# Kernel optimization log

Hardware: AMD Instinct MI355X
Metric: run time of the kernel (lower is better)

The kernel has to match this reference:

```python
import jax, jax.numpy as jnp
import numpy as np

N, E, D, T, B, OUT = 20000, 80000, 768, 4, 3, 768
SCALE = 0.02


def _layer_norm(x, g, b):
    mu = jnp.mean(x, axis=-1, keepdims=True)
    var = jnp.var(x, axis=-1, keepdims=True)
    return (x - mu) / jnp.sqrt(var + 1e-5) * g + b


def _typed_linear(x, etype, bases, coeff):
    # DGL TypedLinear with basis regularizer: W[t] = sum_b coeff[t,b] * bases[b]
    # computed as 3 shared GEMMs + per-edge weighted sum (avoids [E,D,D] gather).
    c = coeff[etype]  # [E, B]
    y = c[:, 0:1] * (x @ bases[0])
    for bb in range(1, bases.shape[0]):
        y = y + c[:, bb:bb + 1] * (x @ bases[bb])
    return y


def _time_encode(t, freq, phase):
    return jnp.cos(t[:, None] * freq[None, :] + phase[None, :])


def _segment_softmax(scores, seg, n):
    m = jax.ops.segment_max(scores, seg, num_segments=n)
    m = jnp.where(jnp.isfinite(m), m, 0.0)  # empty segments -> -inf guard
    e = jnp.exp(scores - m[seg])
    den = jax.ops.segment_sum(e, seg, num_segments=n)[seg]
    return e / jnp.where(den == 0, 1.0, den)


def _forward(h, etime_hete, first_etime_homo, second_etime_homo, w_src, w_dst,
             ln_g, ln_b, src_bases, src_coeff, dst_bases, dst_coeff,
             user_bases, user_coeff, lin_w, lin_b, time_freq, time_phase,
             src_hete, dst_hete, first_etype_hete, src_homo, dst_homo,
             first_etype_homo, second_etype_homo, n_nodes):
    inv_sqrt_d = 1.0 / jnp.sqrt(jnp.asarray(768.0, h.dtype))
    n_src = h @ w_src.T  # src_weight (no bias)
    n_dst = h @ w_dst.T  # dst_weight (no bias)

    # --- heterogeneous edges ---
    sf = n_src[src_hete]
    df = n_dst[dst_hete]
    hete_src = jax.nn.relu(_typed_linear(_layer_norm(sf, ln_g, ln_b), first_etype_hete, src_bases, src_coeff))
    msg_h = _time_encode(etime_hete, time_freq, time_phase) + hete_src
    e_h = jnp.sum(msg_h * df, axis=1) * inv_sqrt_d
    a_h = _segment_softmax(e_h, dst_hete, n_nodes)
    h_hete = jax.ops.segment_sum(a_h[:, None] * msg_h, dst_hete, num_segments=n_nodes)

    # --- homogeneous edges ---
    sf = n_src[src_homo]
    df = n_dst[dst_homo]
    dst_feat = jax.nn.relu(_typed_linear(_layer_norm(df, ln_g, ln_b), first_etype_homo, dst_bases, dst_coeff))
    homo_feat = jax.nn.relu(_typed_linear(_layer_norm(sf, ln_g, ln_b), second_etype_homo, user_bases, user_coeff))
    t_homo = jnp.maximum(first_etime_homo, second_etime_homo)
    msg_o = _time_encode(t_homo, time_freq, time_phase) + homo_feat
    e_o = jnp.sum(msg_o * dst_feat, axis=1) * inv_sqrt_d
    a_o = _segment_softmax(e_o, dst_homo, n_nodes)
    h_homo = jax.ops.segment_sum(a_o[:, None] * msg_o, dst_homo, num_segments=n_nodes)

    n = jnp.concatenate([h_hete, h_homo], axis=-1)  # [N, 2D]
    z = jax.nn.relu(n @ lin_w.T + lin_b)
    zn = jnp.linalg.norm(z, axis=1, keepdims=True)
    return z / jnp.where(zn == 0, 1.0, zn)


def setup_inputs() -> dict:
    key = jax.random.key(0)
    ks = jax.random.split(key, 24)
    inp = {
        'h': jax.random.normal(ks[0], (N, D), jnp.float32),
        'etime_hete': jax.random.uniform(ks[1], (E,), jnp.float32),
        'first_etime_homo': jax.random.uniform(ks[2], (E,), jnp.float32),
        'second_etime_homo': jax.random.uniform(ks[3], (E,), jnp.float32),
        'w_src': jax.random.normal(ks[4], (D, D), jnp.float32) * SCALE,
        'w_dst': jax.random.normal(ks[5], (D, D), jnp.float32) * SCALE,
        'ln_g': jnp.ones((D,), jnp.float32),
        'ln_b': jnp.zeros((D,), jnp.float32),
        'src_bases': jax.random.normal(ks[6], (B, D, D), jnp.float32) * SCALE,
        'src_coeff': jax.random.normal(ks[7], (T, B), jnp.float32),
        'dst_bases': jax.random.normal(ks[8], (B, D, D), jnp.float32) * SCALE,
        'dst_coeff': jax.random.normal(ks[9], (T, B), jnp.float32),
        'user_bases': jax.random.normal(ks[10], (B, D, D), jnp.float32) * SCALE,
        'user_coeff': jax.random.normal(ks[11], (T, B), jnp.float32),
        'lin_w': jax.random.normal(ks[12], (OUT, 2 * D), jnp.float32) * SCALE,
        'lin_b': jnp.zeros((OUT,), jnp.float32),
        'time_freq': jnp.asarray(1.0 / 10 ** np.linspace(0, 9, D), jnp.float32),
        'time_phase': jnp.zeros((D,), jnp.float32),
        'src_hete': jax.random.randint(ks[13], (E,), 0, N, jnp.int32),
        'dst_hete': jax.random.randint(ks[14], (E,), 0, N, jnp.int32),
        'first_etype_hete': jax.random.randint(ks[15], (E,), 0, T, jnp.int32),
        'src_homo': jax.random.randint(ks[16], (E,), 0, N, jnp.int32),
        'dst_homo': jax.random.randint(ks[17], (E,), 0, N, jnp.int32),
        'first_etype_homo': jax.random.randint(ks[18], (E,), 0, T, jnp.int32),
        'second_etype_homo': jax.random.randint(ks[19], (E,), 0, T, jnp.int32),
        'num_nodes': N,
    }
    return inp


def reference(h, etime_hete, first_etime_homo, second_etime_homo, w_src, w_dst,
              ln_g, ln_b, src_bases, src_coeff, dst_bases, dst_coeff,
              user_bases, user_coeff, lin_w, lin_b, time_freq, time_phase,
              src_hete, dst_hete, first_etype_hete, src_homo, dst_homo,
              first_etype_homo, second_etype_homo, num_nodes):
    return _forward(h, etime_hete, first_etime_homo, second_etime_homo, w_src,
                    w_dst, ln_g, ln_b, src_bases, src_coeff, dst_bases,
                    dst_coeff, user_bases, user_coeff, lin_w, lin_b,
                    time_freq, time_phase, src_hete, dst_hete,
                    first_etype_hete, src_homo, dst_homo, first_etype_homo,
                    second_etype_homo, num_nodes)
```

## Files before the change

kernel.cpp:

```cpp
#include <hip/hip_runtime.h>
#include <hip/hip_bf16.h>
#include <stdint.h>

#define D 768
#define INV_SQRT_D 0.03608439182435161269f

static void* g_scratch = nullptr;
#define SCRATCH_BYTES ((size_t)600 * 1024 * 1024)

__attribute__((constructor))
static void _alloc_scratch() {
    if (hipMalloc(&g_scratch, SCRATCH_BYTES) != hipSuccess) g_scratch = nullptr;
}

static inline int cdiv(int a, int b) { return (a + b - 1) / b; }

typedef __attribute__((ext_vector_type(8))) short bf16x8;
typedef __attribute__((ext_vector_type(4))) float f32x4;

__device__ __forceinline__ unsigned cvt2b(float lo, float hi) {
    unsigned r;
    asm("v_cvt_pk_bf16_f32 %0, %1, %2" : "=v"(r) : "v"(lo), "v"(hi));
    return r;
}
__device__ __forceinline__ unsigned short f2b(float f) {
    return (unsigned short)cvt2b(f, f);
}
__device__ __forceinline__ float b2f(unsigned short u) {
    union { unsigned u; float f; } c; c.u = (unsigned)u << 16;
    return c.f;
}

__device__ __forceinline__ float block_reduce_sum(float v) {
#pragma unroll
    for (int off = 32; off > 0; off >>= 1) v += __shfl_down(v, off, 64);
    __shared__ float sm[4];
    int lane = threadIdx.x & 63, w = threadIdx.x >> 6;
    __syncthreads();
    if (lane == 0) sm[w] = v;
    __syncthreads();
    return (sm[0] + sm[1]) + (sm[2] + sm[3]);
}

template <bool CONCAT, bool BF16C, bool RELU, bool BIAS>
__global__ __launch_bounds__(256) void mfma_gemm(
    const unsigned short* __restrict__ A1, const unsigned short* __restrict__ A2,
    int lda, int ksplit,
    const unsigned short* __restrict__ B, int ldb,
    void* __restrict__ Cv, int ldc,
    const float* __restrict__ bias,
    int M, int K)
{
    __shared__ unsigned short As[128 * 64];
    __shared__ unsigned short Bs[128 * 64];
    const int tid = threadIdx.x;
    const int wv = tid >> 6, lane = tid & 63;
    const int m0 = blockIdx.y * 128, n0 = blockIdx.x * 128;
    const int wm = (wv >> 1) << 6;
    const int wn = (wv & 1) << 6;
    const int fr = lane & 15;
    const int fq = lane >> 4;

    f32x4 acc[4][4] = {};

    for (int k0 = 0; k0 < K; k0 += 64) {
        const unsigned short* Asrc = A1;
        int kk = k0;
        if (CONCAT && k0 >= ksplit) { Asrc = A2; kk = k0 - ksplit; }
#pragma unroll
        for (int j = 0; j < 4; ++j) {
            int idx = j * 256 + tid;
            int row = idx >> 3;
            int gs  = ((idx & 7) ^ (row & 7)) << 3;
            int am = m0 + row; if (am > M - 1) am = M - 1;
            const unsigned short* ga = Asrc + (size_t)am * lda + kk + gs;
            char* la = (char*)As + (size_t)(j * 256 + wv * 64) * 16;
            __builtin_amdgcn_global_load_lds(
                (const __attribute__((address_space(1))) unsigned int*)ga,
                (__attribute__((address_space(3))) unsigned int*)la, 16, 0, 0);
            const unsigned short* gb = B + (size_t)(n0 + row) * ldb + k0 + gs;
            char* lb = (char*)Bs + (size_t)(j * 256 + wv * 64) * 16;
            __builtin_amdgcn_global_load_lds(
                (const __attribute__((address_space(1))) unsigned int*)gb,
                (__attribute__((address_space(3))) unsigned int*)lb, 16, 0, 0);
        }
        __syncthreads();

#pragma unroll
        for (int ks = 0; ks < 2; ++ks) {
            bf16x8 af[4], bfv[4];
            const int gr = (((ks * 4 + fq) ^ (fr & 7)) << 3);
#pragma unroll
            for (int i = 0; i < 4; ++i) {
                af[i]  = *(const bf16x8*)&As[(wm + i * 16 + fr) * 64 + gr];
                bfv[i] = *(const bf16x8*)&Bs[(wn + i * 16 + fr) * 64 + gr];
            }
#pragma unroll
            for (int mi = 0; mi < 4; ++mi)
#pragma unroll
                for (int ni = 0; ni < 4; ++ni)
                    acc[mi][ni] = __builtin_amdgcn_mfma_f32_16x16x32_bf16(
                        af[mi], bfv[ni], acc[mi][ni], 0, 0, 0);
        }
        __syncthreads();
    }

#pragma unroll
    for (int mi = 0; mi < 4; ++mi) {
#pragma unroll
        for (int r = 0; r < 4; ++r) {
            int m = m0 + wm + mi * 16 + fq * 4 + r;
            if (m >= M) continue;
#pragma unroll
            for (int ni = 0; ni < 4; ++ni) {
                int n = n0 + wn + ni * 16 + fr;
                float v = acc[mi][ni][r];
                if (BIAS) v += bias[n];
                if (RELU) v = fmaxf(v, 0.f);
                if (BF16C) ((unsigned short*)Cv)[(size_t)m * ldc + n] = f2b(v);
                else       ((float*)Cv)[(size_t)m * ldc + n] = v;
            }
        }
    }
}

__global__ void f32_to_bf16_kernel(const float* __restrict__ in,
                                   unsigned short* __restrict__ out, int n4) {
    int i = blockIdx.x * 256 + threadIdx.x;
    if (i >= n4) return;
    float4 v = *reinterpret_cast<const float4*>(in + (size_t)i * 4);
    ushort4 o;
    o.x = f2b(v.x); o.y = f2b(v.y); o.z = f2b(v.z); o.w = f2b(v.w);
    *reinterpret_cast<ushort4*>(out + (size_t)i * 4) = o;
}

__global__ __launch_bounds__(256) void combine_transpose_kernel(
    const float* __restrict__ in, const float* __restrict__ coeff,
    unsigned short* __restrict__ out) {
    int t = blockIdx.z;
    float c0 = coeff[t * 3 + 0], c1 = coeff[t * 3 + 1], c2 = coeff[t * 3 + 2];
    __shared__ float tile[32][33];
    int bx = blockIdx.x * 32, by = blockIdx.y * 32;
    int tx = threadIdx.x & 31, ty = threadIdx.x >> 5;
#pragma unroll
    for (int i = 0; i < 32; i += 8) {
        size_t idx = (size_t)(by + ty + i) * D + bx + tx;
        tile[ty + i][tx] = c0 * in[idx] + c1 * in[idx + (size_t)D * D]
                         + c2 * in[idx + (size_t)2 * D * D];
    }
    __syncthreads();
    unsigned short* o = out + (size_t)t * D * D;
#pragma unroll
    for (int i = 0; i < 32; i += 8)
        o[(size_t)(bx + ty + i) * D + by + tx] = f2b(tile[tx][ty + i]);
}

__global__ __launch_bounds__(256) void ln_bf16_kernel(
    unsigned short* __restrict__ x, int ld,
    const float* __restrict__ g, const float* __restrict__ b)
{
    unsigned short* r = x + (size_t)blockIdx.x * ld;
    int t = threadIdx.x;
    float v0 = b2f(r[t]), v1 = b2f(r[t + 256]), v2 = b2f(r[t + 512]);
    float s = block_reduce_sum(v0 + v1 + v2);
    float mu = s * (1.f / 768.f);
    float d0 = v0 - mu, d1 = v1 - mu, d2 = v2 - mu;
    float q = block_reduce_sum(d0 * d0 + d1 * d1 + d2 * d2);
    float rstd = 1.f / sqrtf(q * (1.f / 768.f) + 1e-5f);
    r[t]       = f2b(d0 * rstd * g[t]       + b[t]);
    r[t + 256] = f2b(d1 * rstd * g[t + 256] + b[t + 256]);
    r[t + 512] = f2b(d2 * rstd * g[t + 512] + b[t + 512]);
}

__global__ void zero_int_kernel(int* __restrict__ p, int n) {
    int i = blockIdx.x * 256 + threadIdx.x;
    if (i < n) p[i] = 0;
}

__global__ void count2_kernel(const int* __restrict__ dA, const int* __restrict__ dB,
                              int* __restrict__ cntA, int* __restrict__ cntB, int E) {
    int e = blockIdx.x * 256 + threadIdx.x;
    if (e < E) {
        atomicAdd(&cntA[dA[e]], 1);
        atomicAdd(&cntB[dB[e]], 1);
    }
}

__global__ __launch_bounds__(1024) void scan2_kernel(
    const int* __restrict__ cntA, int* __restrict__ offsA,
    const int* __restrict__ cntB, int* __restrict__ offsB, int n)
{
    __shared__ int tmp[1024];
    __shared__ int carry;
    int tid = threadIdx.x;
    for (int g = 0; g < 2; ++g) {
        const int* cnt = g ? cntB : cntA;
        int* offs = g ? offsB : offsA;
        __syncthreads();
        if (tid == 0) carry = 0;
        __syncthreads();
        for (int base = 0; base < n; base += 1024) {
            int idx = base + tid;
            int v = (idx < n) ? cnt[idx] : 0;
            tmp[tid] = v;
            __syncthreads();
            for (int off = 1; off < 1024; off <<= 1) {
                int t = (tid >= off) ? tmp[tid - off] : 0;
                __syncthreads();
                tmp[tid] += t;
                __syncthreads();
            }
            int inc = tmp[tid];
            int c = carry;
            if (idx < n) offs[idx] = c + inc - v;
            __syncthreads();
            if (tid == 0) carry = c + tmp[1023];
            __syncthreads();
        }
        if (tid == 0) offs[n] = carry;
    }
}

__global__ void scatter2_kernel(
    const int* __restrict__ dA, const int* __restrict__ offsA,
    int* __restrict__ curA, int* __restrict__ listA,
    const int* __restrict__ dB, const int* __restrict__ offsB,
    int* __restrict__ curB, int* __restrict__ listB, int E) {
    int e = blockIdx.x * 256 + threadIdx.x;
    if (e < E) {
        int d = dA[e];
        listA[offsA[d] + atomicAdd(&curA[d], 1)] = e;
        d = dB[e];
        listB[offsB[d] + atomicAdd(&curB[d], 1)] = e;
    }
}

template <bool IS_HOMO>
__global__ __launch_bounds__(256) void edge_fused_kernel(
    const int* __restrict__ offs, const int* __restrict__ list,
    const unsigned short* __restrict__ Pmsg, int ldm,
    const unsigned short* __restrict__ Pdst, int ldd,
    const float* __restrict__ t1, const float* __restrict__ t2,
    const int* __restrict__ src,
    const int* __restrict__ etA,
    const int* __restrict__ etB,
    const float* __restrict__ freq, const float* __restrict__ phase,
    unsigned short* __restrict__ out, int nN)
{
    int v = blockIdx.x * 4 + (threadIdx.x >> 6);
    if (v >= nN) return;
    int l = threadIdx.x & 63;
    bool hi = l < 32;

    float frq[16], phs[16];
#pragma unroll
    for (int q = 0; q < 16; ++q) { frq[q] = 0.f; phs[q] = 0.f; }
    {
        float4 f0 = *(const float4*)(freq + l * 8);
        float4 f1 = *(const float4*)(freq + l * 8 + 4);
        float4 p0 = *(const float4*)(phase + l * 8);
        float4 p1 = *(const float4*)(phase + l * 8 + 4);
        frq[0] = f0.x; frq[1] = f0.y; frq[2] = f0.z; frq[3] = f0.w;
        frq[4] = f1.x; frq[5] = f1.y; frq[6] = f1.z; frq[7] = f1.w;
        phs[0] = p0.x; phs[1] = p0.y; phs[2] = p0.z; phs[3] = p0.w;
        phs[4] = p1.x; phs[5] = p1.y; phs[6] = p1.z; phs[7] = p1.w;
    }
    if (hi) {
        float4 f0 = *(const float4*)(freq + 512 + l * 8);
        float4 f1 = *(const float4*)(freq + 512 + l * 8 + 4);
        float4 p0 = *(const float4*)(phase + 512 + l * 8);
        float4 p1 = *(const float4*)(phase + 512 + l * 8 + 4);
        frq[8]  = f0.x; frq[9]  = f0.y; frq[10] = f0.z; frq[11] = f0.w;
        frq[12] = f1.x; frq[13] = f1.y; frq[14] = f1.z; frq[15] = f1.w;
        phs[8]  = p0.x; phs[9]  = p0.y; phs[10] = p0.z; phs[11] = p0.w;
        phs[12] = p1.x; phs[13] = p1.y; phs[14] = p1.z; phs[15] = p1.w;
    }

    float nd[16];
#pragma unroll
    for (int q = 0; q < 16; ++q) nd[q] = 0.f;
    if (!IS_HOMO) {
        const unsigned short* pd = Pdst + (size_t)v * ldd;
        bf16x8 r0 = *(const bf16x8*)(pd + l * 8);
#pragma unroll
        for (int q = 0; q < 8; ++q) nd[q] = b2f((unsigned short)r0[q]);
        if (hi) {
            bf16x8 r1 = *(const bf16x8*)(pd + 512 + l * 8);
#pragma unroll
            for (int q = 0; q < 8; ++q) nd[8 + q] = b2f((unsigned short)r1[q]);
        }
    }

    float m = -INFINITY, den = 0.f;
    float acc[16];
#pragma unroll
    for (int q = 0; q < 16; ++q) acc[q] = 0.f;

    int i0 = offs[v], i1 = offs[v + 1];
    for (int i = i0; i < i1; ++i) {
        int e = list[i];
        int s = src[e];
        float tv = IS_HOMO ? fmaxf(t1[e], t2[e]) : t1[e];
        int tym = IS_HOMO ? etB[e] : etA[e];
        const unsigned short* pm = Pmsg + (size_t)s * ldm + tym * D;

        float msg[16];
#pragma unroll
        for (int q = 0; q < 16; ++q) msg[q] = 0.f;
        bf16x8 r0 = *(const bf16x8*)(pm + l * 8);
#pragma unroll
        for (int q = 0; q < 8; ++q)
            msg[q] = __cosf(tv * frq[q] + phs[q]) + b2f((unsigned short)r0[q]);
        if (hi) {
            bf16x8 r1 = *(const bf16x8*)(pm + 512 + l * 8);
#pragma unroll
            for (int q = 0; q < 8; ++q)
                msg[8 + q] = __cosf(tv * frq[8 + q] + phs[8 + q])
                           + b2f((unsigned short)r1[q]);
        }

        float dotp = 0.f;
        if (IS_HOMO) {
            int ta = etA[e];
            const unsigned short* pd2 = Pdst + (size_t)v * ldd + ta * D;
            bf16x8 d0 = *(const bf16x8*)(pd2 + l * 8);
#pragma unroll
            for (int q = 0; q < 8; ++q)
                dotp += msg[q] * b2f((unsigned short)d0[q]);
            if (hi) {
                bf16x8 d1 = *(const bf16x8*)(pd2 + 512 + l * 8);
#pragma unroll
                for (int q = 0; q < 8; ++q)
                    dotp += msg[8 + q] * b2f((unsigned short)d1[q]);
            }
        } else {
#pragma unroll
            for (int q = 0; q < 16; ++q) dotp += msg[q] * nd[q];
        }
#pragma unroll
        for (int off = 1; off < 64; off <<= 1) dotp += __shfl_xor(dotp, off, 64);
        float sc = dotp * INV_SQRT_D;

        float nm = fmaxf(m, sc);
        float sOld = __expf(m - nm);
        float w = __expf(sc - nm);
        den = den * sOld + w;
#pragma unroll
        for (int q = 0; q < 16; ++q) acc[q] = acc[q] * sOld + w * msg[q];
        m = nm;
    }

    float inv = (den > 0.f) ? 1.f / den : 0.f;
    unsigned short* o = out + (size_t)v * D;
    uint4 st;
    st.x = cvt2b(acc[0] * inv, acc[1] * inv); st.y = cvt2b(acc[2] * inv, acc[3] * inv);
    st.z = cvt2b(acc[4] * inv, acc[5] * inv); st.w = cvt2b(acc[6] * inv, acc[7] * inv);
    *reinterpret_cast<uint4*>(o + (size_t)l * 8) = st;
    if (hi) {
        st.x = cvt2b(acc[8] * inv, acc[9] * inv);   st.y = cvt2b(acc[10] * inv, acc[11] * inv);
        st.z = cvt2b(acc[12] * inv, acc[13] * inv); st.w = cvt2b(acc[14] * inv, acc[15] * inv);
        *reinterpret_cast<uint4*>(o + 512 + (size_t)l * 8) = st;
    }
}

__global__ __launch_bounds__(256) void normalize_kernel(
    const float* __restrict__ z, float* __restrict__ out)
{
    const float* x = z + (size_t)blockIdx.x * D;
    int t = threadIdx.x;
    float v0 = x[t], v1 = x[t + 256], v2 = x[t + 512];
    float s = block_reduce_sum(v0 * v0 + v1 * v1 + v2 * v2);
    float nrm = sqrtf(s);
    float inv = (nrm == 0.f) ? 1.f : 1.f / nrm;
    float* o = out + (size_t)blockIdx.x * D;
    o[t] = v0 * inv; o[t + 256] = v1 * inv; o[t + 512] = v2 * inv;
}

__global__ void fill_f32_kernel(float* __restrict__ p, float v, int n) {
    int i = blockIdx.x * 256 + threadIdx.x;
    if (i < n) p[i] = v;
}

extern "C" void kernel_launch(void* const* d_in, const int* in_sizes, int n_in,
                              void* d_out, int out_size, void* d_ws, size_t ws_size,
                              hipStream_t stream)
{
    const float* h          = (const float*)d_in[0];
    const float* etime_hete = (const float*)d_in[1];
    const float* t1_homo    = (const float*)d_in[2];
    const float* t2_homo    = (const float*)d_in[3];
    const float* w_src      = (const float*)d_in[4];
    const float* w_dst      = (const float*)d_in[5];
    const float* ln_g       = (const float*)d_in[6];
    const float* ln_b       = (const float*)d_in[7];
    const float* src_bases  = (const float*)d_in[8];
    const float* src_coeff  = (const float*)d_in[9];
    const float* dst_bases  = (const float*)d_in[10];
    const float* dst_coeff  = (const float*)d_in[11];
    const float* user_bases = (const float*)d_in[12];
    const float* user_coeff = (const float*)d_in[13];
    const float* lin_w      = (const float*)d_in[14];
    const float* lin_b      = (const float*)d_in[15];
    const float* time_freq  = (const float*)d_in[16];
    const float* time_phase = (const float*)d_in[17];
    const int* src_hete = (const int*)d_in[18];
    const int* dst_hete = (const int*)d_in[19];
    const int* et_hete  = (const int*)d_in[20];
    const int* src_homo = (const int*)d_in[21];
    const int* dst_homo = (const int*)d_in[22];
    const int* et1_homo = (const int*)d_in[23];
    const int* et2_homo = (const int*)d_in[24];

    const int N = in_sizes[0] / D;
    const int E = in_sizes[1];

    const size_t szST  = (size_t)N * 1536 * 2;
    const size_t szPSU = (size_t)N * 6144 * 2;
    const size_t szPD  = (size_t)N * 3072 * 2;
    const size_t szVb  = (size_t)N * D * 2;
    const size_t szW   = (size_t)D * D * 2;
    size_t need = szST + szPSU + szPD + 3 * szVb
                + 2 * szW + 2 * szW + 8 * szW + 4 * szW
                + (size_t)2 * N * 4
                + 2 * (((size_t)(N + 1) * 4 + 255) & ~(size_t)255)
                + (size_t)2 * E * 4 + 16384;

    char* base;
    if (ws_size >= need) base = (char*)d_ws;
    else if (g_scratch)  base = (char*)g_scratch;
    else {
        fill_f32_kernel<<<cdiv(out_size, 256), 256, 0, stream>>>(
            (float*)d_out, 1000.0f + (float)(ws_size >> 20), out_size);
        return;
    }

    char* p = base;
    auto carve = [&](size_t bytes) { char* r = p; p += (bytes + 255) & ~(size_t)255; return r; };
    unsigned short* STb = (unsigned short*)carve(szST);
    unsigned short* PSU = (unsigned short*)carve(szPSU);
    unsigned short* PD  = (unsigned short*)carve(szPD);
    unsigned short* hb  = (unsigned short*)carve(szVb);
    unsigned short* hAb = (unsigned short*)carve(szVb);
    unsigned short* hOb = (unsigned short*)carve(szVb);
    unsigned short* wsb = (unsigned short*)carve(2 * szW);
    unsigned short* lwb = (unsigned short*)carve(2 * szW);
    unsigned short* suW = (unsigned short*)carve(8 * szW);
    unsigned short* dstW = (unsigned short*)carve(4 * szW);
    int* cnt    = (int*)carve((size_t)2 * N * 4);
    int* offsA  = (int*)carve((size_t)(N + 1) * 4);
    int* offsB  = (int*)carve((size_t)(N + 1) * 4);
    int* listA  = (int*)carve((size_t)E * 4);
    int* listB  = (int*)carve((size_t)E * 4);
    float* z    = (float*)PSU;

    unsigned short* Sb = STb;
    unsigned short* Tb = STb + 768;
    unsigned short* Psrc_t  = PSU;
    unsigned short* Puser_t = PSU + 3072;

    const int eb = cdiv(E, 256);
    const int nb2 = cdiv(2 * N, 256);
    const int MB = cdiv(N, 128);
    dim3 g_proj(12, MB);
    dim3 g_psu(48, MB);
    dim3 g_pd(24, MB);
    dim3 g_fin(6, MB);
    dim3 ct_grid(24, 24, 4);
    const int agb = cdiv(N, 4);

    f32_to_bf16_kernel<<<cdiv(N * D / 4, 256), 256, 0, stream>>>(h, hb, N * D / 4);
    f32_to_bf16_kernel<<<cdiv(D * D / 4, 256), 256, 0, stream>>>(w_src, wsb, D * D / 4);
    f32_to_bf16_kernel<<<cdiv(D * D / 4, 256), 256, 0, stream>>>(w_dst, wsb + (size_t)D * D, D * D / 4);
    f32_to_bf16_kernel<<<cdiv(D * 2 * D / 4, 256), 256, 0, stream>>>(lin_w, lwb, D * 2 * D / 4);
    combine_transpose_kernel<<<ct_grid, 256, 0, stream>>>(src_bases, src_coeff, suW);
    combine_transpose_kernel<<<ct_grid, 256, 0, stream>>>(user_bases, user_coeff, suW + (size_t)4 * D * D);
    combine_transpose_kernel<<<ct_grid, 256, 0, stream>>>(dst_bases, dst_coeff, dstW);

    zero_int_kernel<<<nb2, 256, 0, stream>>>(cnt, 2 * N);
    count2_kernel<<<eb, 256, 0, stream>>>(dst_hete, dst_homo, cnt, cnt + N, E);
    scan2_kernel<<<1, 1024, 0, stream>>>(cnt, offsA, cnt + N, offsB, N);
    zero_int_kernel<<<nb2, 256, 0, stream>>>(cnt, 2 * N);
    scatter2_kernel<<<eb, 256, 0, stream>>>(dst_hete, offsA, cnt, listA,
                                            dst_homo, offsB, cnt + N, listB, E);

    mfma_gemm<false, true, false, false><<<g_proj, 256, 0, stream>>>(
        hb, hb, D, D, wsb, D, STb, 1536, nullptr, N, D);
    ln_bf16_kernel<<<N, 256, 0, stream>>>(Sb, 1536, ln_g, ln_b);

    mfma_gemm<false, true, true, false><<<g_psu, 256, 0, stream>>>(
        Sb, Sb, 1536, D, suW, D, PSU, 6144, nullptr, N, D);

    edge_fused_kernel<false><<<agb, 256, 0, stream>>>(
        offsA, listA, Psrc_t, 6144, Tb, 1536,
        etime_hete, nullptr, src_hete, et_hete, nullptr,
        time_freq, time_phase, hAb, N);

    ln_bf16_kernel<<<N, 256, 0, stream>>>(Tb, 1536, ln_g, ln_b);
    mfma_gemm<false, true, true, false><<<g_pd, 256, 0, stream>>>(
        Tb, Tb, 1536, D, dstW, D, PD, 3072, nullptr, N, D);

    edge_fused_kernel<true><<<agb, 256, 0, stream>>>(
        offsB, listB, Puser_t, 6144, PD, 3072,
        t1_homo, t2_homo, src_homo, et1_homo, et2_homo,
        time_freq, time_phase, hOb, N);

    mfma_gemm<true, false, true, true><<<g_fin, 256, 0, stream>>>(
        hAb, hOb, D, D, lwb, 2 * D, z, D, lin_b, N, 2 * D);
    normalize_kernel<<<N, 256, 0, stream>>>(z, (float*)d_out);
}
```

Baseline: 1.002 ms.

## Software-pipeline edge gathers in attention kernel and hoist GEMM load addressing

The per-node edge attention loop now prefetches message and destination feature rows two edges ahead, and edge metadata three ahead, using rotating registers. This hides the latency of the dependent gathers behind the online-softmax math. Separately, the GEMM precomputes its global and LDS load pointers once and bumps them each K step, switching to A2 at the split point. The cost is higher register pressure, and the LDS write layout changes from per-wave to per-thread offsets.

```diff
diff --git a/kernel.cpp b/kernel.cpp
--- a/kernel.cpp
+++ b/kernel.cpp
@@ -61,28 +61,44 @@
     const int fr = lane & 15;
     const int fq = lane >> 4;
 
+    const int rtid = tid >> 3;
+    const int ctid = tid & 7;
+    const unsigned short* ga[4];
+    const unsigned short* gb[4];
+    char* la[4];
+    char* lb[4];
+#pragma unroll
+    for (int j = 0; j < 4; ++j) {
+        int row = j * 32 + rtid;
+        int gs  = (ctid ^ (row & 7)) << 3;
+        int am = m0 + row; if (am > M - 1) am = M - 1;
+        ga[j] = A1 + (size_t)am * lda + gs;
+        gb[j] = B + (size_t)(n0 + row) * ldb + gs;
+        la[j] = (char*)As + (size_t)(j * 256 + tid) * 16;
+        lb[j] = (char*)Bs + (size_t)(j * 256 + tid) * 16;
+    }
+
     f32x4 acc[4][4] = {};
 
     for (int k0 = 0; k0 < K; k0 += 64) {
-        const unsigned short* Asrc = A1;
-        int kk = k0;
-        if (CONCAT && k0 >= ksplit) { Asrc = A2; kk = k0 - ksplit; }
+        if (CONCAT && k0 == ksplit) {
+#pragma unroll
+            for (int j = 0; j < 4; ++j) {
+                int row = j * 32 + rtid;
+                int gs  = (ctid ^ (row & 7)) << 3;
+                int am = m0 + row; if (am > M - 1) am = M - 1;
+                ga[j] = A2 + (size_t)am * lda + gs;
+            }
+        }
 #pragma unroll
         for (int j = 0; j < 4; ++j) {
-            int idx = j * 256 + tid;
-            int row = idx >> 3;
-            int gs  = ((idx & 7) ^ (row & 7)) << 3;
-            int am = m0 + row; if (am > M - 1) am = M - 1;
-            const unsigned short* ga = Asrc + (size_t)am * lda + kk + gs;
-            char* la = (char*)As + (size_t)(j * 256 + wv * 64) * 16;
             __builtin_amdgcn_global_load_lds(
-                (const __attribute__((address_space(1))) unsigned int*)ga,
-                (__attribute__((address_space(3))) unsigned int*)la, 16, 0, 0);
-            const unsigned short* gb = B + (size_t)(n0 + row) * ldb + k0 + gs;
-            char* lb = (char*)Bs + (size_t)(j * 256 + wv * 64) * 16;
+                (const __attribute__((address_space(1))) unsigned int*)ga[j],
+                (__attribute__((address_space(3))) unsigned int*)la[j], 16, 0, 0);
             __builtin_amdgcn_global_load_lds(
-                (const __attribute__((address_space(1))) unsigned int*)gb,
-                (__attribute__((address_space(3))) unsigned int*)lb, 16, 0, 0);
+                (const __attribute__((address_space(1))) unsigned int*)gb[j],
+                (__attribute__((address_space(3))) unsigned int*)lb[j], 16, 0, 0);
+            ga[j] += 64; gb[j] += 64;
         }
         __syncthreads();
 
@@ -297,41 +313,81 @@
     for (int q = 0; q < 16; ++q) acc[q] = 0.f;
 
     int i0 = offs[v], i1 = offs[v + 1];
+
+    auto loadmeta = [&](int i, int& s_, float& tv_, int& tym_, int& ta_) {
+        int e = list[i];
+        s_ = src[e];
+        tv_ = IS_HOMO ? fmaxf(t1[e], t2[e]) : t1[e];
+        tym_ = IS_HOMO ? etB[e] : etA[e];
+        if (IS_HOMO) ta_ = etA[e];
+    };
+
+    float tvC = 0.f, tvN = 0.f, tvX = 0.f;
+    int sX = 0, tymX = 0, taX = 0;
+    bf16x8 mC0 = {}, mC1 = {}, dC0 = {}, dC1 = {};
+    bf16x8 mN0 = {}, mN1 = {}, dN0 = {}, dN1 = {};
+
+    if (i0 < i1) {
+        int s_, tym_, ta_ = 0;
+        loadmeta(i0, s_, tvC, tym_, ta_);
+        const unsigned short* pm = Pmsg + (size_t)s_ * ldm + tym_ * D;
+        mC0 = *(const bf16x8*)(pm + l * 8);
+        if (hi) mC1 = *(const bf16x8*)(pm + 512 + l * 8);
+        if (IS_HOMO) {
+            const unsigned short* pd2 = Pdst + (size_t)v * ldd + ta_ * D;
+            dC0 = *(const bf16x8*)(pd2 + l * 8);
+            if (hi) dC1 = *(const bf16x8*)(pd2 + 512 + l * 8);
+        }
+    }
+    if (i0 + 1 < i1) {
+        int s_, tym_, ta_ = 0;
+        loadmeta(i0 + 1, s_, tvN, tym_, ta_);
+        const unsigned short* pm = Pmsg + (size_t)s_ * ldm + tym_ * D;
+        mN0 = *(const bf16x8*)(pm + l * 8);
+        if (hi) mN1 = *(const bf16x8*)(pm + 512 + l * 8);
+        if (IS_HOMO) {
+            const unsigned short* pd2 = Pdst + (size_t)v * ldd + ta_ * D;
+            dN0 = *(const bf16x8*)(pd2 + l * 8);
+            if (hi) dN1 = *(const bf16x8*)(pd2 + 512 + l * 8);
+        }
+    }
+    if (i0 + 2 < i1) loadmeta(i0 + 2, sX, tvX, tymX, taX);
+
     for (int i = i0; i < i1; ++i) {
-        int e = list[i];
-        int s = src[e];
-        float tv = IS_HOMO ? fmaxf(t1[e], t2[e]) : t1[e];
-        int tym = IS_HOMO ? etB[e] : etA[e];
-        const unsigned short* pm = Pmsg + (size_t)s * ldm + tym * D;
+        bf16x8 mX0 = {}, mX1 = {}, dX0 = {}, dX1 = {};
+        float tvXcur = tvX;
+        int sXn = 0, tymXn = 0, taXn = 0; float tvXn = 0.f;
+        if (i + 2 < i1) {
+            const unsigned short* pm = Pmsg + (size_t)sX * ldm + tymX * D;
+            mX0 = *(const bf16x8*)(pm + l * 8);
+            if (hi) mX1 = *(const bf16x8*)(pm + 512 + l * 8);
+            if (IS_HOMO) {
+                const unsigned short* pd2 = Pdst + (size_t)v * ldd + taX * D;
+                dX0 = *(const bf16x8*)(pd2 + l * 8);
+                if (hi) dX1 = *(const bf16x8*)(pd2 + 512 + l * 8);
+            }
+            if (i + 3 < i1) loadmeta(i + 3, sXn, tvXn, tymXn, taXn);
+        }
 
         float msg[16];
 #pragma unroll
-        for (int q = 0; q < 16; ++q) msg[q] = 0.f;
-        bf16x8 r0 = *(const bf16x8*)(pm + l * 8);
-#pragma unroll
         for (int q = 0; q < 8; ++q)
-            msg[q] = __cosf(tv * frq[q] + phs[q]) + b2f((unsigned short)r0[q]);
-        if (hi) {
-            bf16x8 r1 = *(const bf16x8*)(pm + 512 + l * 8);
-#pragma unroll
-            for (int q = 0; q < 8; ++q)
-                msg[8 + q] = __cosf(tv * frq[8 + q] + phs[8 + q])
-                           + b2f((unsigned short)r1[q]);
-        }
+            msg[q] = __cosf(tvC * frq[q] + phs[q]) + b2f((unsigned short)mC0[q]);
+#pragma unroll
+        for (int q = 0; q < 8; ++q)
+            msg[8 + q] = hi ? (__cosf(tvC * frq[8 + q] + phs[8 + q])
+                               + b2f((unsigned short)mC1[q]))
+                            : 0.f;
 
         float dotp = 0.f;
         if (IS_HOMO) {
-            int ta = etA[e];
-            const unsigned short* pd2 = Pdst + (size_t)v * ldd + ta * D;
-            bf16x8 d0 = *(const bf16x8*)(pd2 + l * 8);
 #pragma unroll
             for (int q = 0; q < 8; ++q)
-                dotp += msg[q] * b2f((unsigned short)d0[q]);
+                dotp += msg[q] * b2f((unsigned short)dC0[q]);
             if (hi) {
-                bf16x8 d1 = *(const bf16x8*)(pd2 + 512 + l * 8);
 #pragma unroll
                 for (int q = 0; q < 8; ++q)
-                    dotp += msg[8 + q] * b2f((unsigned short)d1[q]);
+                    dotp += msg[8 + q] * b2f((unsigned short)dC1[q]);
             }
         } else {
 #pragma unroll
@@ -348,6 +404,10 @@
 #pragma unroll
         for (int q = 0; q < 16; ++q) acc[q] = acc[q] * sOld + w * msg[q];
         m = nm;
+
+        mC0 = mN0; mC1 = mN1; dC0 = dN0; dC1 = dN1; tvC = tvN;
+        mN0 = mX0; mN1 = mX1; dN0 = dX0; dN1 = dX1; tvN = tvXcur;
+        sX = sXn; tvX = tvXn; tymX = tymXn; taX = taXn;
     }
 
     float inv = (den > 0.f) ? 1.f / den : 0.f;
```

Measured after the change: 1.014 ms. Within noise of the previous version (+1.3%).
